# Performance work log

Hardware: AMD Instinct MI355X
Metric: run time of the kernel (lower is better)

Reference implementation:

```python
import jax, jax.numpy as jnp
import numpy as np

E, D_MODEL, D_HIDDEN, N_TOKENS = 8, 1024, 4096, 16384


def setup_inputs() -> dict:
    key = jax.random.key(0)
    ks = jax.random.split(key, 6)
    inp = {
        "hidden_states": jax.random.normal(ks[0], (N_TOKENS, D_MODEL), jnp.float32),
        # tokens are pre-sorted by expert; equal-sized groups of N_TOKENS // E
        "fwd_expert_count": jnp.full((E,), N_TOKENS // E, dtype=jnp.int32),
        # weights stored [E, d_in, d_out] (math-equivalent transpose of torch's [E, out, in])
        "w_gelu": jax.random.normal(ks[1], (E, D_MODEL, D_HIDDEN), jnp.float32) * 0.02,
        "w_lin": jax.random.normal(ks[2], (E, D_MODEL, D_HIDDEN), jnp.float32) * 0.02,
        "b_lin": jax.random.normal(ks[3], (E, D_HIDDEN), jnp.float32) * 0.02,
        "w_o": jax.random.normal(ks[4], (E, D_HIDDEN, D_MODEL), jnp.float32) * 0.02,
        "b_o": jax.random.normal(ks[5], (E, D_MODEL), jnp.float32) * 0.02,
    }
    return inp


def reference(hidden_states, fwd_expert_count, w_gelu, w_lin, b_lin, w_o, b_o):
    # Grouped GEMM MoE expert FFN with gated GELU (T5DenseGatedActDense per expert).
    # setup_inputs uses equal group sizes, so the grouped GEMM is expressed as a
    # batched einsum over [E, capacity, d] blocks (tokens are sorted by expert).
    e, d_model, d_hidden = w_gelu.shape
    n = hidden_states.shape[0]
    cap = n // e  # per-expert token count (== fwd_expert_count[i])
    x = hidden_states.reshape(e, cap, d_model)
    # gate branch: no bias (FMoELinear bias=False), gelu_new (tanh approx)
    hidden_gelu = jax.nn.gelu(jnp.einsum('ecd,edh->ech', x, w_gelu), approximate=True)
    # linear branch: bias=True
    hidden_linear = jnp.einsum('ecd,edh->ech', x, w_lin) + b_lin[:, None, :]
    h = hidden_gelu * hidden_linear  # dropout is identity at inference
    out = jnp.einsum('ech,ehd->ecd', h, w_o) + b_o[:, None, :]
    return out.reshape(n, d_model)
```

## Files before the change

kernel.cpp:

```cpp
#include <hip/hip_runtime.h>

#define EXP 8
#define DM 1024
#define DH 4096
#define NT 16384

typedef __attribute__((ext_vector_type(8))) short bf16x8;
typedef __attribute__((ext_vector_type(16))) float f32x16;

static __device__ __forceinline__ unsigned short f2bf(float f) {
  unsigned int u = __float_as_uint(f);
  u = u + 0x7FFFu + ((u >> 16) & 1u);
  return (unsigned short)(u >> 16);
}

static __device__ __forceinline__ void gload_lds16(const void* g, void* l) {
  __builtin_amdgcn_global_load_lds((const __attribute__((address_space(1))) void*)g,
                                   (__attribute__((address_space(3))) void*)l, 16, 0, 0);
}

__global__ void cvt_bf16_k(const float* __restrict__ in, unsigned short* __restrict__ out,
                           long n4) {
  long i = (long)blockIdx.x * blockDim.x + threadIdx.x;
  const long stride = (long)gridDim.x * blockDim.x;
  for (; i < n4; i += stride) {
    const float4 v = ((const float4*)in)[i];
    ushort4 o;
    o.x = f2bf(v.x); o.y = f2bf(v.y); o.z = f2bf(v.z); o.w = f2bf(v.w);
    ((ushort4*)out)[i] = o;
  }
}

__global__ void transpose_cvt(const float* __restrict__ in, unsigned short* __restrict__ out,
                              int K, int N) {
  __shared__ float tile[32][33];
  const int n0 = blockIdx.x * 32, k0 = blockIdx.y * 32;
  const size_t boff = (size_t)blockIdx.z * K * N;
  const int tx = threadIdx.x, ty = threadIdx.y;
  const float* src = in + boff;
  unsigned short* dst = out + boff;
#pragma unroll
  for (int i = 0; i < 32; i += 8)
    tile[ty + i][tx] = src[(size_t)(k0 + ty + i) * N + n0 + tx];
  __syncthreads();
#pragma unroll
  for (int i = 0; i < 32; i += 8)
    dst[(size_t)(n0 + ty + i) * K + k0 + tx] = f2bf(tile[tx][ty + i]);
}


__global__ __launch_bounds__(256, 2) void gemm1(
    const unsigned short* __restrict__ Xb,
    const unsigned short* __restrict__ WgT,
    const unsigned short* __restrict__ WlT,
    const float* __restrict__ b_lin,
    unsigned short* __restrict__ Hb) {
  __shared__ unsigned short sA[256 * 64];
  __shared__ unsigned short sBg[64 * 64];
  __shared__ unsigned short sBl[64 * 64];

  const int t = threadIdx.x;
  const int nblk = blockIdx.x;
  const int mblk = blockIdx.y;
  const int e = mblk >> 3;
  const int m0 = mblk * 256, n0 = nblk * 64;

  const int lane = t & 63, wave = t >> 6;
  const int wr = wave >> 1, wh = wave & 1;
  const int lr = lane & 31, kg = lane >> 5;
  const int cx = lr & 7;

  const int srow = t >> 3;
  const int csw = ((t & 7) ^ (srow & 7)) << 3;
  const unsigned short* gA = Xb + (size_t)(m0 + srow) * DM + csw;
  const unsigned short* gG = WgT + ((size_t)e * DH + n0 + srow) * DM + csw;
  const unsigned short* gL = WlT + ((size_t)e * DH + n0 + srow) * DM + csw;

  f32x16 accg[4], accl[4];
#pragma unroll
  for (int m = 0; m < 4; m++) { accg[m] = 0.0f; accl[m] = 0.0f; }

  int rbA[4];
#pragma unroll
  for (int m = 0; m < 4; m++) rbA[m] = (wr * 128 + m * 32 + lr) * 64;
  const int rbB = (wh * 32 + lr) * 64;

  for (int kt = 0; kt < DM / 64; ++kt) {
    const int k0 = kt * 64;
#pragma unroll
    for (int i = 0; i < 8; i++)
      gload_lds16(gA + (size_t)(i * 32) * DM + k0,
                  (char*)sA + (i * 32 + srow) * 128 + (t & 7) * 16);
#pragma unroll
    for (int i = 0; i < 2; i++) {
      gload_lds16(gG + (size_t)(i * 32) * DM + k0,
                  (char*)sBg + (i * 32 + srow) * 128 + (t & 7) * 16);
      gload_lds16(gL + (size_t)(i * 32) * DM + k0,
                  (char*)sBl + (i * 32 + srow) * 128 + (t & 7) * 16);
    }
    __syncthreads();
#pragma unroll
    for (int ks = 0; ks < 4; ks++) {
      const int co = ((ks * 2 + kg) ^ cx) << 3;
      bf16x8 af[4];
#pragma unroll
      for (int m = 0; m < 4; m++) af[m] = *(const bf16x8*)&sA[rbA[m] + co];
      const bf16x8 bg = *(const bf16x8*)&sBg[rbB + co];
      const bf16x8 bl = *(const bf16x8*)&sBl[rbB + co];
#pragma unroll
      for (int m = 0; m < 4; m++) {
        accg[m] = __builtin_amdgcn_mfma_f32_32x32x16_bf16(af[m], bg, accg[m], 0, 0, 0);
        accl[m] = __builtin_amdgcn_mfma_f32_32x32x16_bf16(af[m], bl, accl[m], 0, 0, 0);
      }
    }
    __syncthreads();
  }

  const int gcol = n0 + wh * 32 + lr;
  const float bias = b_lin[(size_t)e * DH + gcol];
#pragma unroll
  for (int m = 0; m < 4; m++) {
    const int base = m0 + wr * 128 + m * 32 + 4 * kg;
#pragma unroll
    for (int r = 0; r < 16; r++) {
      const int grow = base + (r & 3) + 8 * (r >> 2);
      const float g = accg[m][r];
      const float li = accl[m][r] + bias;
      const float u = 0.7978845608028654f * (g + 0.044715f * g * g * g);
      const float th = 1.0f - 2.0f / (1.0f + __expf(2.0f * u));
      const float h = 0.5f * g * (1.0f + th) * li;
      Hb[(size_t)grow * DH + gcol] = f2bf(h);
    }
  }
}

__global__ __launch_bounds__(256, 2) void gemm2(
    const unsigned short* __restrict__ Hb,
    const unsigned short* __restrict__ WoT,
    const float* __restrict__ b_o,
    float* __restrict__ out) {
  __shared__ unsigned short sA[256 * 64];
  __shared__ unsigned short sB[128 * 64];

  const int t = threadIdx.x;
  const int nblk = blockIdx.x;
  const int mblk = blockIdx.y;
  const int e = mblk >> 3;
  const int m0 = mblk * 256, n0 = nblk * 128;

  const int lane = t & 63, wave = t >> 6;
  const int wr = wave >> 1, wn = wave & 1;
  const int lr = lane & 31, kg = lane >> 5;
  const int cx = lr & 7;

  const int srow = t >> 3;
  const int csw = ((t & 7) ^ (srow & 7)) << 3;
  const unsigned short* gA = Hb + (size_t)(m0 + srow) * DH + csw;
  const unsigned short* gB = WoT + ((size_t)e * DM + n0 + srow) * DH + csw;

  f32x16 acc[4][2];
#pragma unroll
  for (int m = 0; m < 4; m++)
#pragma unroll
    for (int n = 0; n < 2; n++) acc[m][n] = 0.0f;

  int rbA[4];
#pragma unroll
  for (int m = 0; m < 4; m++) rbA[m] = (wr * 128 + m * 32 + lr) * 64;
  int rbB[2];
#pragma unroll
  for (int n = 0; n < 2; n++) rbB[n] = (wn * 64 + n * 32 + lr) * 64;

  for (int kt = 0; kt < DH / 64; ++kt) {
    const int k0 = kt * 64;
#pragma unroll
    for (int i = 0; i < 8; i++)
      gload_lds16(gA + (size_t)(i * 32) * DH + k0,
                  (char*)sA + (i * 32 + srow) * 128 + (t & 7) * 16);
#pragma unroll
    for (int i = 0; i < 4; i++)
      gload_lds16(gB + (size_t)(i * 32) * DH + k0,
                  (char*)sB + (i * 32 + srow) * 128 + (t & 7) * 16);
    __syncthreads();
#pragma unroll
    for (int ks = 0; ks < 4; ks++) {
      const int co = ((ks * 2 + kg) ^ cx) << 3;
      bf16x8 af[4], bf[2];
#pragma unroll
      for (int m = 0; m < 4; m++) af[m] = *(const bf16x8*)&sA[rbA[m] + co];
#pragma unroll
      for (int n = 0; n < 2; n++) bf[n] = *(const bf16x8*)&sB[rbB[n] + co];
#pragma unroll
      for (int m = 0; m < 4; m++)
#pragma unroll
        for (int n = 0; n < 2; n++)
          acc[m][n] = __builtin_amdgcn_mfma_f32_32x32x16_bf16(af[m], bf[n], acc[m][n], 0, 0, 0);
    }
    __syncthreads();
  }

  const float* bop = b_o + (size_t)e * DM;
#pragma unroll
  for (int n = 0; n < 2; n++) {
    const int gcol = n0 + wn * 64 + n * 32 + lr;
    const float bias = bop[gcol];
#pragma unroll
    for (int m = 0; m < 4; m++) {
      const int base = m0 + wr * 128 + m * 32 + 4 * kg;
#pragma unroll
      for (int r = 0; r < 16; r++) {
        const int grow = base + (r & 3) + 8 * (r >> 2);
        out[(size_t)grow * DM + gcol] = acc[m][n][r] + bias;
      }
    }
  }
}

extern "C" void kernel_launch(void* const* d_in, const int* in_sizes, int n_in,
                              void* d_out, int out_size, void* d_ws, size_t ws_size,
                              hipStream_t stream) {
  const float* hs = (const float*)d_in[0];
  const float* w_gelu = (const float*)d_in[2];
  const float* w_lin = (const float*)d_in[3];
  const float* b_lin = (const float*)d_in[4];
  const float* w_o = (const float*)d_in[5];
  const float* b_o = (const float*)d_in[6];
  float* outp = (float*)d_out;

  unsigned short* Xb = (unsigned short*)d_ws;
  unsigned short* WgT = Xb + (size_t)NT * DM;
  unsigned short* WlT = WgT + (size_t)EXP * DH * DM;
  unsigned short* WoT = WlT + (size_t)EXP * DH * DM;
  unsigned short* Hb = WoT + (size_t)EXP * DH * DM;

  cvt_bf16_k<<<dim3(2048), dim3(256), 0, stream>>>(hs, Xb, (long)NT * DM / 4);
  transpose_cvt<<<dim3(DH / 32, DM / 32, EXP), dim3(32, 8), 0, stream>>>(w_gelu, WgT, DM, DH);
  transpose_cvt<<<dim3(DH / 32, DM / 32, EXP), dim3(32, 8), 0, stream>>>(w_lin, WlT, DM, DH);
  transpose_cvt<<<dim3(DM / 32, DH / 32, EXP), dim3(32, 8), 0, stream>>>(w_o, WoT, DH, DM);

  gemm1<<<dim3(DH / 64, NT / 256), dim3(256), 0, stream>>>(Xb, WgT, WlT, b_lin, Hb);
  gemm2<<<dim3(DM / 128, NT / 256), dim3(256), 0, stream>>>(Hb, WoT, b_o, outp);
}
```

Before: 652.4 us.

## Pipeline both expert GEMMs with double-buffered LDS, register prefetch and 512-thread tiles

Both GEMM kernels are rewritten to use 512-thread blocks with 256x256 output tiles (gate and linear columns interleaved in gemm1), a two-stage LDS ring fed by async global-to-LDS loads, and register-level prefetch of the next K-tile's MFMA fragments. The single per-tile __syncthreads pair is replaced by explicit vmcnt/lgkmcnt waits and per-phase barriers, with s_setprio raised around the MFMA bursts. The grid is reordered to M-major. The goal is to hide global and LDS latency behind matrix math and to raise reuse per tile. In exchange it uses 128 KB of LDS and many fragment registers per block, which limits occupancy to one block per CU.

```diff
diff --git a/kernel.cpp b/kernel.cpp
--- a/kernel.cpp
+++ b/kernel.cpp
@@ -49,74 +49,111 @@
 }
 
 
-__global__ __launch_bounds__(256, 2) void gemm1(
+__global__ __launch_bounds__(512, 1) void gemm1(
     const unsigned short* __restrict__ Xb,
     const unsigned short* __restrict__ WgT,
     const unsigned short* __restrict__ WlT,
     const float* __restrict__ b_lin,
     unsigned short* __restrict__ Hb) {
-  __shared__ unsigned short sA[256 * 64];
-  __shared__ unsigned short sBg[64 * 64];
-  __shared__ unsigned short sBl[64 * 64];
+  __shared__ unsigned short lds[2 * 32768];
 
   const int t = threadIdx.x;
-  const int nblk = blockIdx.x;
-  const int mblk = blockIdx.y;
+  const int mblk = blockIdx.x, nblk = blockIdx.y;
   const int e = mblk >> 3;
-  const int m0 = mblk * 256, n0 = nblk * 64;
+  const int m0 = mblk * 256, n0 = nblk * 128;
 
   const int lane = t & 63, wave = t >> 6;
-  const int wr = wave >> 1, wh = wave & 1;
+  const int wr = wave >> 2, wc = wave & 3;
   const int lr = lane & 31, kg = lane >> 5;
-  const int cx = lr & 7;
-
-  const int srow = t >> 3;
-  const int csw = ((t & 7) ^ (srow & 7)) << 3;
-  const unsigned short* gA = Xb + (size_t)(m0 + srow) * DM + csw;
-  const unsigned short* gG = WgT + ((size_t)e * DH + n0 + srow) * DM + csw;
-  const unsigned short* gL = WlT + ((size_t)e * DH + n0 + srow) * DM + csw;
-
-  f32x16 accg[4], accl[4];
-#pragma unroll
-  for (int m = 0; m < 4; m++) { accg[m] = 0.0f; accl[m] = 0.0f; }
-
-  int rbA[4];
-#pragma unroll
-  for (int m = 0; m < 4; m++) rbA[m] = (wr * 128 + m * 32 + lr) * 64;
-  const int rbB = (wh * 32 + lr) * 64;
-
-  for (int kt = 0; kt < DM / 64; ++kt) {
-    const int k0 = kt * 64;
-#pragma unroll
-    for (int i = 0; i < 8; i++)
-      gload_lds16(gA + (size_t)(i * 32) * DM + k0,
-                  (char*)sA + (i * 32 + srow) * 128 + (t & 7) * 16);
-#pragma unroll
-    for (int i = 0; i < 2; i++) {
-      gload_lds16(gG + (size_t)(i * 32) * DM + k0,
-                  (char*)sBg + (i * 32 + srow) * 128 + (t & 7) * 16);
-      gload_lds16(gL + (size_t)(i * 32) * DM + k0,
-                  (char*)sBl + (i * 32 + srow) * 128 + (t & 7) * 16);
-    }
-    __syncthreads();
-#pragma unroll
-    for (int ks = 0; ks < 4; ks++) {
-      const int co = ((ks * 2 + kg) ^ cx) << 3;
-      bf16x8 af[4];
-#pragma unroll
-      for (int m = 0; m < 4; m++) af[m] = *(const bf16x8*)&sA[rbA[m] + co];
-      const bf16x8 bg = *(const bf16x8*)&sBg[rbB + co];
-      const bf16x8 bl = *(const bf16x8*)&sBl[rbB + co];
-#pragma unroll
-      for (int m = 0; m < 4; m++) {
-        accg[m] = __builtin_amdgcn_mfma_f32_32x32x16_bf16(af[m], bg, accg[m], 0, 0, 0);
-        accl[m] = __builtin_amdgcn_mfma_f32_32x32x16_bf16(af[m], bl, accl[m], 0, 0, 0);
+
+  const int srow = t >> 2;
+  const int sch8 = ((t & 3) ^ ((srow >> 1) & 3)) * 8;
+  const unsigned short* gA = Xb + (size_t)(m0 + srow) * DM + sch8;
+  const unsigned short* gG = WgT + ((size_t)e * DH + n0 + srow) * DM + sch8;
+  const unsigned short* gL = WlT + ((size_t)e * DH + n0 + srow) * DM + sch8;
+
+  const int KT = DM / 64;
+
+  auto STAGE = [&](int T2, int u) {
+    unsigned short* d = &lds[(T2 & 1) * 32768 + u * 8192 + t * 8];
+    const int ko = T2 * 64 + (u >> 1) * 32;
+    if (u & 1) {
+      gload_lds16(gG + ko, d);
+      gload_lds16(gL + ko, d + 4096);
+    } else {
+      gload_lds16(gA + ko, d);
+      gload_lds16(gA + (size_t)128 * DM + ko, d + 4096);
+    }
+  };
+
+  f32x16 acc[4][2];
+#pragma unroll
+  for (int m = 0; m < 4; m++)
+#pragma unroll
+    for (int n = 0; n < 2; n++) acc[m][n] = 0.0f;
+
+  bf16x8 fA[4][4], fB[2][4];
+
+  int rowA[4], rowB[2];
+#pragma unroll
+  for (int m = 0; m < 4; m++) rowA[m] = wr * 128 + m * 32 + lr;
+  rowB[0] = wc * 32 + lr;
+  rowB[1] = 128 + wc * 32 + lr;
+
+#pragma unroll
+  for (int u = 0; u < 4; u++) STAGE(0, u);
+#pragma unroll
+  for (int u = 0; u < 4; u++) STAGE(1, u);
+  asm volatile("s_waitcnt vmcnt(4)" ::: "memory");
+  __builtin_amdgcn_s_barrier();
+  __builtin_amdgcn_sched_barrier(0);
+#pragma unroll
+  for (int p = 0; p < 4; p++) {
+    const unsigned short* bA = &lds[(p >> 1) * 16384];
+    const unsigned short* bB = bA + 8192;
+#pragma unroll
+    for (int m = 0; m < 4; m++)
+      fA[m][p] = *(const bf16x8*)&bA[rowA[m] * 32 + ((((p & 1) * 2 + kg) ^ ((rowA[m] >> 1) & 3)) * 8)];
+#pragma unroll
+    for (int n = 0; n < 2; n++)
+      fB[n][p] = *(const bf16x8*)&bB[rowB[n] * 32 + ((((p & 1) * 2 + kg) ^ ((rowB[n] >> 1) & 3)) * 8)];
+  }
+  asm volatile("s_waitcnt lgkmcnt(0)" ::: "memory");
+  __builtin_amdgcn_s_barrier();
+  __builtin_amdgcn_sched_barrier(0);
+
+  for (int T = 0; T < KT; ++T) {
+    const int rs = (T + 1) & 1;
+#pragma unroll
+    for (int p = 0; p < 4; p++) {
+      __builtin_amdgcn_s_setprio(1);
+#pragma unroll
+      for (int m = 0; m < 4; m++)
+#pragma unroll
+        for (int n = 0; n < 2; n++)
+          acc[m][n] = __builtin_amdgcn_mfma_f32_32x32x16_bf16(fA[m][p], fB[n][p], acc[m][n], 0, 0, 0);
+      __builtin_amdgcn_s_setprio(0);
+      if (T + 2 < KT) STAGE(T + 2, p);
+      if (T + 1 < KT) {
+        const unsigned short* bA = &lds[rs * 32768 + (p >> 1) * 16384];
+        const unsigned short* bB = bA + 8192;
+#pragma unroll
+        for (int m = 0; m < 4; m++)
+          fA[m][p] = *(const bf16x8*)&bA[rowA[m] * 32 + ((((p & 1) * 2 + kg) ^ ((rowA[m] >> 1) & 3)) * 8)];
+#pragma unroll
+        for (int n = 0; n < 2; n++)
+          fB[n][p] = *(const bf16x8*)&bB[rowB[n] * 32 + ((((p & 1) * 2 + kg) ^ ((rowB[n] >> 1) & 3)) * 8)];
+        if (p == 1 || p == 3) {
+          if (T + 2 < KT) asm volatile("s_waitcnt vmcnt(4)" ::: "memory");
+          else            asm volatile("s_waitcnt vmcnt(0)" ::: "memory");
+        }
       }
-    }
-    __syncthreads();
-  }
-
-  const int gcol = n0 + wh * 32 + lr;
+      __builtin_amdgcn_s_barrier();
+      __builtin_amdgcn_sched_barrier(0);
+    }
+  }
+
+  const int gcol = n0 + wc * 32 + lr;
   const float bias = b_lin[(size_t)e * DH + gcol];
 #pragma unroll
   for (int m = 0; m < 4; m++) {
@@ -124,8 +161,8 @@
 #pragma unroll
     for (int r = 0; r < 16; r++) {
       const int grow = base + (r & 3) + 8 * (r >> 2);
-      const float g = accg[m][r];
-      const float li = accl[m][r] + bias;
+      const float g = acc[m][0][r];
+      const float li = acc[m][1][r] + bias;
       const float u = 0.7978845608028654f * (g + 0.044715f * g * g * g);
       const float th = 1.0f - 2.0f / (1.0f + __expf(2.0f * u));
       const float h = 0.5f * g * (1.0f + th) * li;
@@ -134,29 +171,40 @@
   }
 }
 
-__global__ __launch_bounds__(256, 2) void gemm2(
+__global__ __launch_bounds__(512, 1) void gemm2(
     const unsigned short* __restrict__ Hb,
     const unsigned short* __restrict__ WoT,
     const float* __restrict__ b_o,
     float* __restrict__ out) {
-  __shared__ unsigned short sA[256 * 64];
-  __shared__ unsigned short sB[128 * 64];
+  __shared__ unsigned short lds[2 * 32768];
 
   const int t = threadIdx.x;
-  const int nblk = blockIdx.x;
-  const int mblk = blockIdx.y;
+  const int mblk = blockIdx.x, nblk = blockIdx.y;
   const int e = mblk >> 3;
-  const int m0 = mblk * 256, n0 = nblk * 128;
+  const int m0 = mblk * 256, n0 = nblk * 256;
 
   const int lane = t & 63, wave = t >> 6;
-  const int wr = wave >> 1, wn = wave & 1;
+  const int wr = wave >> 2, wc = wave & 3;
   const int lr = lane & 31, kg = lane >> 5;
-  const int cx = lr & 7;
-
-  const int srow = t >> 3;
-  const int csw = ((t & 7) ^ (srow & 7)) << 3;
-  const unsigned short* gA = Hb + (size_t)(m0 + srow) * DH + csw;
-  const unsigned short* gB = WoT + ((size_t)e * DM + n0 + srow) * DH + csw;
+
+  const int srow = t >> 2;
+  const int sch8 = ((t & 3) ^ ((srow >> 1) & 3)) * 8;
+  const unsigned short* gA = Hb + (size_t)(m0 + srow) * DH + sch8;
+  const unsigned short* gB = WoT + ((size_t)e * DM + n0 + srow) * DH + sch8;
+
+  const int KT = DH / 64;
+
+  auto STAGE = [&](int T2, int u) {
+    unsigned short* d = &lds[(T2 & 1) * 32768 + u * 8192 + t * 8];
+    const int ko = T2 * 64 + (u >> 1) * 32;
+    if (u & 1) {
+      gload_lds16(gB + ko, d);
+      gload_lds16(gB + (size_t)128 * DH + ko, d + 4096);
+    } else {
+      gload_lds16(gA + ko, d);
+      gload_lds16(gA + (size_t)128 * DH + ko, d + 4096);
+    }
+  };
 
   f32x16 acc[4][2];
 #pragma unroll
@@ -164,45 +212,71 @@
 #pragma unroll
     for (int n = 0; n < 2; n++) acc[m][n] = 0.0f;
 
-  int rbA[4];
-#pragma unroll
-  for (int m = 0; m < 4; m++) rbA[m] = (wr * 128 + m * 32 + lr) * 64;
-  int rbB[2];
-#pragma unroll
-  for (int n = 0; n < 2; n++) rbB[n] = (wn * 64 + n * 32 + lr) * 64;
-
-  for (int kt = 0; kt < DH / 64; ++kt) {
-    const int k0 = kt * 64;
-#pragma unroll
-    for (int i = 0; i < 8; i++)
-      gload_lds16(gA + (size_t)(i * 32) * DH + k0,
-                  (char*)sA + (i * 32 + srow) * 128 + (t & 7) * 16);
-#pragma unroll
-    for (int i = 0; i < 4; i++)
-      gload_lds16(gB + (size_t)(i * 32) * DH + k0,
-                  (char*)sB + (i * 32 + srow) * 128 + (t & 7) * 16);
-    __syncthreads();
-#pragma unroll
-    for (int ks = 0; ks < 4; ks++) {
-      const int co = ((ks * 2 + kg) ^ cx) << 3;
-      bf16x8 af[4], bf[2];
-#pragma unroll
-      for (int m = 0; m < 4; m++) af[m] = *(const bf16x8*)&sA[rbA[m] + co];
-#pragma unroll
-      for (int n = 0; n < 2; n++) bf[n] = *(const bf16x8*)&sB[rbB[n] + co];
+  bf16x8 fA[4][4], fB[2][4];
+
+  int rowA[4], rowB[2];
+#pragma unroll
+  for (int m = 0; m < 4; m++) rowA[m] = wr * 128 + m * 32 + lr;
+#pragma unroll
+  for (int n = 0; n < 2; n++) rowB[n] = wc * 64 + n * 32 + lr;
+
+#pragma unroll
+  for (int u = 0; u < 4; u++) STAGE(0, u);
+#pragma unroll
+  for (int u = 0; u < 4; u++) STAGE(1, u);
+  asm volatile("s_waitcnt vmcnt(4)" ::: "memory");
+  __builtin_amdgcn_s_barrier();
+  __builtin_amdgcn_sched_barrier(0);
+#pragma unroll
+  for (int p = 0; p < 4; p++) {
+    const unsigned short* bA = &lds[(p >> 1) * 16384];
+    const unsigned short* bB = bA + 8192;
+#pragma unroll
+    for (int m = 0; m < 4; m++)
+      fA[m][p] = *(const bf16x8*)&bA[rowA[m] * 32 + ((((p & 1) * 2 + kg) ^ ((rowA[m] >> 1) & 3)) * 8)];
+#pragma unroll
+    for (int n = 0; n < 2; n++)
+      fB[n][p] = *(const bf16x8*)&bB[rowB[n] * 32 + ((((p & 1) * 2 + kg) ^ ((rowB[n] >> 1) & 3)) * 8)];
+  }
+  asm volatile("s_waitcnt lgkmcnt(0)" ::: "memory");
+  __builtin_amdgcn_s_barrier();
+  __builtin_amdgcn_sched_barrier(0);
+
+  for (int T = 0; T < KT; ++T) {
+    const int rs = (T + 1) & 1;
+#pragma unroll
+    for (int p = 0; p < 4; p++) {
+      __builtin_amdgcn_s_setprio(1);
 #pragma unroll
       for (int m = 0; m < 4; m++)
 #pragma unroll
         for (int n = 0; n < 2; n++)
-          acc[m][n] = __builtin_amdgcn_mfma_f32_32x32x16_bf16(af[m], bf[n], acc[m][n], 0, 0, 0);
-    }
-    __syncthreads();
+          acc[m][n] = __builtin_amdgcn_mfma_f32_32x32x16_bf16(fA[m][p], fB[n][p], acc[m][n], 0, 0, 0);
+      __builtin_amdgcn_s_setprio(0);
+      if (T + 2 < KT) STAGE(T + 2, p);
+      if (T + 1 < KT) {
+        const unsigned short* bA = &lds[rs * 32768 + (p >> 1) * 16384];
+        const unsigned short* bB = bA + 8192;
+#pragma unroll
+        for (int m = 0; m < 4; m++)
+          fA[m][p] = *(const bf16x8*)&bA[rowA[m] * 32 + ((((p & 1) * 2 + kg) ^ ((rowA[m] >> 1) & 3)) * 8)];
+#pragma unroll
+        for (int n = 0; n < 2; n++)
+          fB[n][p] = *(const bf16x8*)&bB[rowB[n] * 32 + ((((p & 1) * 2 + kg) ^ ((rowB[n] >> 1) & 3)) * 8)];
+        if (p == 1 || p == 3) {
+          if (T + 2 < KT) asm volatile("s_waitcnt vmcnt(4)" ::: "memory");
+          else            asm volatile("s_waitcnt vmcnt(0)" ::: "memory");
+        }
+      }
+      __builtin_amdgcn_s_barrier();
+      __builtin_amdgcn_sched_barrier(0);
+    }
   }
 
   const float* bop = b_o + (size_t)e * DM;
 #pragma unroll
   for (int n = 0; n < 2; n++) {
-    const int gcol = n0 + wn * 64 + n * 32 + lr;
+    const int gcol = n0 + wc * 64 + n * 32 + lr;
     const float bias = bop[gcol];
 #pragma unroll
     for (int m = 0; m < 4; m++) {
@@ -238,6 +312,6 @@
   transpose_cvt<<<dim3(DH / 32, DM / 32, EXP), dim3(32, 8), 0, stream>>>(w_lin, WlT, DM, DH);
   transpose_cvt<<<dim3(DM / 32, DH / 32, EXP), dim3(32, 8), 0, stream>>>(w_o, WoT, DH, DM);
 
-  gemm1<<<dim3(DH / 64, NT / 256), dim3(256), 0, stream>>>(Xb, WgT, WlT, b_lin, Hb);
-  gemm2<<<dim3(DM / 128, NT / 256), dim3(256), 0, stream>>>(Hb, WoT, b_o, outp);
-}
+  gemm1<<<dim3(NT / 256, DH / 128), dim3(512), 0, stream>>>(Xb, WgT, WlT, b_lin, Hb);
+  gemm2<<<dim3(NT / 256, DM / 256), dim3(512), 0, stream>>>(Hb, WoT, b_o, outp);
+}
```

Measured after the change: 721.9 us. +10.6%, slower.
